# Optimization experiments

Hardware: AMD Instinct MI355X
Metric: run time of the kernel (lower is better)

The kernel has to match this reference:

```python
import jax, jax.numpy as jnp
import numpy as np

BS, L, D = 4, 2048, 1024
H, E, K = 8, 16, 2
HD = D // H            # 128
I = 4096 // H          # 512 per-expert intermediate


def setup_inputs() -> dict:
    key = jax.random.key(0)
    ks = jax.random.split(key, 10)
    s = lambda k, shp, fan: jax.random.normal(k, shp, jnp.float32) / np.sqrt(fan)
    return {
        "x": jax.random.normal(ks[0], (BS, L, D), jnp.float32),
        "Wm": s(ks[1], (D, D), D),
        "bm": jnp.zeros((D,), jnp.float32),
        "expert_emb": jax.random.normal(ks[2], (HD, E), jnp.float32),
        "W1": s(ks[3], (E, HD, I), HD),
        "b1": jnp.zeros((E, I), jnp.float32),
        "W2": s(ks[4], (E, I, HD), I),
        "b2": jnp.zeros((E, HD), jnp.float32),
        "Wo": s(ks[5], (D, D), D),
        "bo": jnp.zeros((D,), jnp.float32),
    }


def reference(x, Wm, bm, expert_emb, W1, b1, W2, b2, Wo, bo):
    bs, L_, d = x.shape
    # multi_head projection then split each token into H sub-tokens of HD dims
    h = x @ Wm + bm                              # [bs, L, d]
    t = h.reshape(bs * L_ * H, HD)               # [T, HD], T = bs*L*H
    # routing per sub-token
    logits = t @ expert_emb                      # [T, E]
    w = jax.nn.softmax(logits, axis=-1)
    topw, topi = jax.lax.top_k(w, K)             # [T, K]
    # dense all-experts MLP (faithful to torch.stack over all experts)
    hmid = jax.nn.gelu(jnp.einsum('td,edi->tei', t, W1) + b1, approximate=False)  # [T, E, I]
    eo = jnp.einsum('tei,eio->teo', hmid, W2) + b2                                # [T, E, HD]
    # gather top-k expert outputs and combine with router weights
    sel = jnp.take_along_axis(eo, topi[:, :, None], axis=1)   # [T, K, HD]
    comb = (sel * topw[:, :, None]).sum(axis=1)               # [T, HD]
    out = comb.reshape(bs, L_, d)
    return out @ Wo + bo
```

## Files before the change

### kernel.cpp

```cpp
#include <hip/hip_runtime.h>
#include <hip/hip_bf16.h>
#include <math.h>

typedef __attribute__((ext_vector_type(8))) short bx8;
typedef __attribute__((ext_vector_type(4))) short sx4;
typedef __attribute__((ext_vector_type(4))) float fx4;

#define D_   1024
#define H_   8
#define E_   16
#define HD_  128
#define I_   512
#define M8_  8192
#define T_   65536

__device__ inline float bf2f(short u) {
  unsigned int x = ((unsigned int)(unsigned short)u) << 16;
  return __builtin_bit_cast(float, x);
}
__device__ inline short f2bf(float f) {
  __hip_bfloat16 h = __float2bfloat16(f);
  return __builtin_bit_cast(short, h);
}

__device__ inline void gload_lds16(const void* g, void* l) {
  __builtin_amdgcn_global_load_lds(
      (const __attribute__((address_space(1))) void*)g,
      (__attribute__((address_space(3))) void*)l, 16, 0, 0);
}

__device__ inline fx4 mfma16(bx8 a, bx8 b, fx4 c) {
  return __builtin_amdgcn_mfma_f32_16x16x32_bf16(a, b, c, 0, 0, 0);
}

__device__ inline float gelu_erf(float x) {
  float z = fabsf(x) * 0.70710678118654752f;
  float t = __builtin_amdgcn_rcpf(fmaf(0.3275911f, z, 1.f));
  float p = t * fmaf(t, fmaf(t, fmaf(t, fmaf(t, 1.061405429f, -1.453152027f),
                                     1.421413741f), -0.284496736f), 0.254829592f);
  float er = fmaf(-p, __expf(-z * z), 1.f);
  er = copysignf(er, x);
  return 0.5f * x * (1.f + er);
}


__global__ __launch_bounds__(256) void cvt_bf16_k(const float* __restrict__ src,
                                                  __hip_bfloat16* __restrict__ dst) {
  int i = blockIdx.x * 256 + threadIdx.x;
  float4 v = *(const float4*)&src[(size_t)i * 4];
  sx4 o;
  o[0] = f2bf(v.x); o[1] = f2bf(v.y); o[2] = f2bf(v.z); o[3] = f2bf(v.w);
  *(sx4*)((short*)dst + (size_t)i * 4) = o;
}

__global__ __launch_bounds__(256) void tcvt(const float* __restrict__ src,
                                            __hip_bfloat16* __restrict__ dst,
                                            int R, int C) {
  __shared__ float tile[32][33];
  int tx = threadIdx.x & 31, ty = threadIdx.x >> 5;
  int r0 = blockIdx.y * 32, c0 = blockIdx.x * 32;
  const float* s = src + (size_t)blockIdx.z * R * C;
  __hip_bfloat16* d = dst + (size_t)blockIdx.z * R * C;
#pragma unroll
  for (int i = ty; i < 32; i += 8) tile[i][tx] = s[(size_t)(r0 + i) * C + c0 + tx];
  __syncthreads();
#pragma unroll
  for (int i = ty; i < 32; i += 8)
    d[(size_t)(c0 + i) * R + r0 + tx] = __float2bfloat16(tile[tx][i]);
}


__global__ __launch_bounds__(128) void build_wre(const float* __restrict__ Wm,
                                                 const float* __restrict__ bm,
                                                 const float* __restrict__ emb,
                                                 float* __restrict__ Wre,
                                                 float* __restrict__ rbias) {
  __shared__ float wrow[1024];
  __shared__ float embs[2048];
  int tid = threadIdx.x;
  int d = blockIdx.x;
  for (int i = tid; i < 2048; i += 128) embs[i] = emb[i];
  for (int i = tid; i < 1024; i += 128) wrow[i] = Wm[(size_t)d * 1024 + i];
  __syncthreads();
  int eta = tid >> 4, e = tid & 15;
  float acc = 0.f;
  for (int c = 0; c < 128; ++c) acc = fmaf(wrow[eta * 128 + c], embs[c * 16 + e], acc);
  Wre[(size_t)d * 128 + tid] = acc;
  if (blockIdx.x == 0) {
    float b = 0.f;
    for (int c = 0; c < 128; ++c) b = fmaf(bm[eta * 128 + c], embs[c * 16 + e], b);
    rbias[tid] = b;
  }
}

__global__ __launch_bounds__(256) void route_gemm(const float* __restrict__ x,
                                                  const float* __restrict__ Wre,
                                                  const float* __restrict__ rbias,
                                                  float* __restrict__ logits) {
  __shared__ float xs[32][128];
  int tid = threadIdx.x;
  int n = tid & 127, half = tid >> 7;
  int row0 = blockIdx.x * 32;
  float acc[16];
#pragma unroll
  for (int i = 0; i < 16; ++i) acc[i] = 0.f;
  for (int k0 = 0; k0 < 1024; k0 += 128) {
    __syncthreads();
#pragma unroll
    for (int j = 0; j < 4; ++j) {
      int i4 = tid * 4 + j * 1024;
      int row = i4 >> 7, col = i4 & 127;
      *(float4*)&xs[row][col] = *(const float4*)&x[(size_t)(row0 + row) * 1024 + k0 + col];
    }
    __syncthreads();
    for (int d4 = 0; d4 < 128; d4 += 4) {
      float w0 = Wre[(size_t)(k0 + d4 + 0) * 128 + n];
      float w1 = Wre[(size_t)(k0 + d4 + 1) * 128 + n];
      float w2 = Wre[(size_t)(k0 + d4 + 2) * 128 + n];
      float w3 = Wre[(size_t)(k0 + d4 + 3) * 128 + n];
#pragma unroll
      for (int i = 0; i < 16; ++i) {
        float4 xv = *(const float4*)&xs[half * 16 + i][d4];
        acc[i] = fmaf(xv.x, w0, acc[i]);
        acc[i] = fmaf(xv.y, w1, acc[i]);
        acc[i] = fmaf(xv.z, w2, acc[i]);
        acc[i] = fmaf(xv.w, w3, acc[i]);
      }
    }
  }
  float rb = rbias[n];
#pragma unroll
  for (int i = 0; i < 16; ++i)
    logits[(size_t)(row0 + half * 16 + i) * 128 + n] = acc[i] + rb;
}

__global__ __launch_bounds__(256) void route_topk(const float* __restrict__ logits,
                                                  float* __restrict__ topw,
                                                  int* __restrict__ list,
                                                  int* __restrict__ cnt) {
  __shared__ int lcnt[16];
  __shared__ int gbase[16];
  int tid = threadIdx.x;
  if (tid < 16) lcnt[tid] = 0;
  __syncthreads();
  int s = blockIdx.x * 256 + tid;
  const float* lp = logits + (size_t)(s >> 3) * 128 + (s & 7) * 16;
  float v[16];
#pragma unroll
  for (int j = 0; j < 4; ++j) {
    float4 t = *(const float4*)&lp[j * 4];
    v[j * 4 + 0] = t.x; v[j * 4 + 1] = t.y; v[j * 4 + 2] = t.z; v[j * 4 + 3] = t.w;
  }
  float v1 = -1e30f, v2 = -1e30f; int i1 = 0, i2 = 0;
#pragma unroll
  for (int e = 0; e < 16; ++e) {
    float val = v[e];
    if (val > v1) { v2 = v1; i2 = i1; v1 = val; i1 = e; }
    else if (val > v2) { v2 = val; i2 = e; }
  }
  float sum = 0.f;
#pragma unroll
  for (int e = 0; e < 16; ++e) sum += expf(v[e] - v1);
  topw[(size_t)2 * s + 0] = 1.0f / sum;
  topw[(size_t)2 * s + 1] = expf(v2 - v1) / sum;
  int lp1 = atomicAdd(&lcnt[i1], 1);
  int lp2 = atomicAdd(&lcnt[i2], 1);
  __syncthreads();
  if (tid < 16) gbase[tid] = atomicAdd(&cnt[tid], lcnt[tid]);
  __syncthreads();
  list[(size_t)i1 * T_ + gbase[i1] + lp1] = 2 * s;
  list[(size_t)i2 * T_ + gbase[i2] + lp2] = 2 * s + 1;
}

__global__ void prefix_k(const int* __restrict__ cnt, int* __restrict__ tileBase) {
  if (threadIdx.x == 0 && blockIdx.x == 0) {
    int s = 0;
#pragma unroll
    for (int e = 0; e < 16; ++e) { tileBase[e] = s; s += (cnt[e] + 63) >> 6; }
    tileBase[16] = s;
  }
}


template <int OUTF32>
__global__ __launch_bounds__(256) void gemm_bt(const __hip_bfloat16* __restrict__ A,
                                               const __hip_bfloat16* __restrict__ BT,
                                               const float* __restrict__ bias,
                                               void* __restrict__ Cout,
                                               int M, int N, int Kd) {
  __shared__ __hip_bfloat16 As[128 * 64];
  __shared__ __hip_bfloat16 Bs[128 * 64];
  int tid = threadIdx.x;
  int lane = tid & 63, w = tid >> 6;
  int nbn = N >> 7;
  int cpx = gridDim.x >> 3;
  int swz = (blockIdx.x & 7) * cpx + (blockIdx.x >> 3);
  int bm = swz / nbn, bn = swz % nbn;
  int wm = w >> 1, wn = w & 1;
  int r = lane & 15, g = lane >> 4;
  const fx4 fz = {0.f, 0.f, 0.f, 0.f};
  fx4 acc[4][4];
#pragma unroll
  for (int m = 0; m < 4; ++m)
#pragma unroll
    for (int n = 0; n < 4; ++n) acc[m][n] = fz;
  const short* AsS = (const short*)As;
  const short* BsS = (const short*)Bs;
  for (int k0 = 0; k0 < Kd; k0 += 64) {
    __syncthreads();
#pragma unroll
    for (int i = 0; i < 4; ++i) {
      int c = i * 256 + w * 64 + lane;
      int row = c >> 3, ko = (c & 7) * 8;
      gload_lds16(A + (size_t)(bm * 128 + row) * Kd + k0 + ko,
                  (void*)(As + (size_t)(i * 256 + w * 64) * 8));
    }
#pragma unroll
    for (int i = 0; i < 4; ++i) {
      int c = i * 256 + w * 64 + lane;
      int row = c >> 3, ko = (c & 7) * 8;
      gload_lds16(BT + (size_t)(bn * 128 + row) * Kd + k0 + ko,
                  (void*)(Bs + (size_t)(i * 256 + w * 64) * 8));
    }
    __syncthreads();
#pragma unroll
    for (int kb = 0; kb < 2; ++kb) {
      bx8 af[4], bfr[4];
#pragma unroll
      for (int m = 0; m < 4; ++m)
        af[m] = *(const bx8*)(AsS + (wm * 64 + m * 16 + r) * 64 + kb * 32 + g * 8);
#pragma unroll
      for (int n = 0; n < 4; ++n)
        bfr[n] = *(const bx8*)(BsS + (wn * 64 + n * 16 + r) * 64 + kb * 32 + g * 8);
#pragma unroll
      for (int m = 0; m < 4; ++m)
#pragma unroll
        for (int n = 0; n < 4; ++n)
          acc[m][n] = mfma16(af[m], bfr[n], acc[m][n]);
    }
  }
#pragma unroll
  for (int n = 0; n < 4; ++n) {
    int col = bn * 128 + wn * 64 + n * 16 + r;
    float bv = bias[col];
#pragma unroll
    for (int m = 0; m < 4; ++m) {
      int rowb = bm * 128 + wm * 64 + m * 16 + g * 4;
#pragma unroll
      for (int ri = 0; ri < 4; ++ri) {
        float val = acc[m][n][ri] + bv;
        if (OUTF32) ((float*)Cout)[(size_t)(rowb + ri) * N + col] = val;
        else ((__hip_bfloat16*)Cout)[(size_t)(rowb + ri) * N + col] = __float2bfloat16(val);
      }
    }
  }
}


__global__ __launch_bounds__(256, 4) void expert_mlp3(
    const __hip_bfloat16* __restrict__ h,
    const __hip_bfloat16* __restrict__ W1T,
    const __hip_bfloat16* __restrict__ W2T,
    const float* __restrict__ b1,
    const float* __restrict__ b2,
    const float* __restrict__ topw,
    const int* __restrict__ list,
    const int* __restrict__ cnt,
    const int* __restrict__ tileBase,
    __hip_bfloat16* __restrict__ eo) {
  int b = blockIdx.x;
  if (b >= tileBase[16]) return;
  int e = 0;
#pragma unroll
  for (int i = 1; i < 16; ++i) e += (b >= tileBase[i]);
  int tile = b - tileBase[e];
  int cnt_e = cnt[e];
  int base = tile * 64;
  if (base >= cnt_e) return;

  __shared__ short W1c[64 * 128];
  __shared__ short W2c[128 * 64];
  __shared__ short Hc[4 * 16 * 64];

  int tid = threadIdx.x, lane = tid & 63, wv = tid >> 6;
  int r = lane & 15, g = lane >> 4;
  const int* liste = list + (size_t)e * T_;

  int idx_own = base + wv * 16 + r;
  int p_own = (idx_own < cnt_e) ? liste[idx_own] : -1;
  const short* hS = (const short*)h;
  size_t st = (p_own >= 0) ? (size_t)(p_own >> 1) : 0;
  const short* rp = hS + st * 128 + g * 8;
  bx8 af[4];
#pragma unroll
  for (int kb = 0; kb < 4; ++kb) af[kb] = *(const bx8*)(rp + kb * 32);

  const char* W1S = (const char*)(W1T + (size_t)e * I_ * HD_);
  const char* W2S = (const char*)(W2T + (size_t)e * HD_ * I_);
  const float* b1e = b1 + (size_t)e * I_;
  const float* b2e = b2 + (size_t)e * HD_;
  char* HcW = (char*)Hc + wv * 16 * 128;

  const fx4 fz = {0.f, 0.f, 0.f, 0.f};
  fx4 acc2[8];
#pragma unroll
  for (int n = 0; n < 8; ++n) acc2[n] = fz;

  for (int c = 0; c < 8; ++c) {
    __syncthreads();
#pragma unroll
    for (int j = 0; j < 4; ++j) {
      int row = wv * 16 + j * 4 + (lane >> 4);
      int u = lane & 15;
      gload_lds16(W1S + (size_t)(c * 64 + row) * 256 + ((u * 16) ^ ((row & 7) << 4)),
                  (char*)W1c + (wv * 16 + j * 4) * 256);
    }
#pragma unroll
    for (int j = 0; j < 4; ++j) {
      int row = wv * 32 + j * 8 + (lane >> 3);
      int u = lane & 7;
      gload_lds16(W2S + (size_t)row * 1024 + c * 128 + ((u * 16) ^ ((row & 7) << 4)),
                  (char*)W2c + (wv * 32 + j * 8) * 128);
    }
    __syncthreads();

    fx4 acc1[4];
#pragma unroll
    for (int ib = 0; ib < 4; ++ib) acc1[ib] = fz;
#pragma unroll
    for (int kb = 0; kb < 4; ++kb) {
#pragma unroll
      for (int ib = 0; ib < 4; ++ib) {
        int irow = ib * 16 + r;
        bx8 a = *(const bx8*)((const char*)W1c + irow * 256 +
                              ((kb * 64 + g * 16) ^ ((irow & 7) << 4)));
        acc1[ib] = mfma16(a, af[kb], acc1[ib]);
      }
    }

#pragma unroll
    for (int ib = 0; ib < 4; ++ib) {
      float4 b1v = *(const float4*)&b1e[c * 64 + ib * 16 + g * 4];
      sx4 ov;
      ov[0] = f2bf(gelu_erf(acc1[ib][0] + b1v.x));
      ov[1] = f2bf(gelu_erf(acc1[ib][1] + b1v.y));
      ov[2] = f2bf(gelu_erf(acc1[ib][2] + b1v.z));
      ov[3] = f2bf(gelu_erf(acc1[ib][3] + b1v.w));
      *(sx4*)(HcW + r * 128 + ((ib * 32 + g * 8) ^ ((r & 7) << 4))) = ov;
    }

#pragma unroll
    for (int kb2 = 0; kb2 < 2; ++kb2) {
      bx8 ha = *(const bx8*)(HcW + r * 128 + ((kb2 * 64 + g * 16) ^ ((r & 7) << 4)));
#pragma unroll
      for (int ob = 0; ob < 8; ++ob) {
        int orow = ob * 16 + r;
        bx8 wb = *(const bx8*)((const char*)W2c + orow * 128 +
                               ((kb2 * 64 + g * 16) ^ ((orow & 7) << 4)));
        acc2[ob] = mfma16(ha, wb, acc2[ob]);
      }
    }
  }

  int pid_ep[4];
  float wt_ep[4];
#pragma unroll
  for (int ri = 0; ri < 4; ++ri) {
    int idx = base + wv * 16 + g * 4 + ri;
    int p = (idx < cnt_e) ? liste[idx] : -1;
    pid_ep[ri] = p;
    wt_ep[ri] = (p >= 0) ? topw[p] : 0.f;
  }
#pragma unroll
  for (int ob = 0; ob < 8; ++ob) {
    float b2v = b2e[ob * 16 + r];
#pragma unroll
    for (int ri = 0; ri < 4; ++ri) {
      int p = pid_ep[ri];
      if (p >= 0) {
        float v = (acc2[ob][ri] + b2v) * wt_ep[ri];
        eo[(size_t)p * 128 + ob * 16 + r] = __float2bfloat16(v);
      }
    }
  }
}

__global__ __launch_bounds__(256) void combine_k(const __hip_bfloat16* __restrict__ eo,
                                                 __hip_bfloat16* __restrict__ comb) {
  int t = blockIdx.x * 256 + threadIdx.x;
  int s = t >> 4, oo = (t & 15) * 8;
  const short* eS = (const short*)eo;
  bx8 a = *(const bx8*)(eS + (size_t)s * 256 + oo);
  bx8 b = *(const bx8*)(eS + (size_t)s * 256 + 128 + oo);
  bx8 ov;
#pragma unroll
  for (int j = 0; j < 8; ++j) ov[j] = f2bf(bf2f(a[j]) + bf2f(b[j]));
  *(bx8*)((short*)comb + (size_t)s * 128 + oo) = ov;
}


extern "C" void kernel_launch(void* const* d_in, const int* in_sizes, int n_in,
                              void* d_out, int out_size, void* d_ws, size_t ws_size,
                              hipStream_t stream) {
  const float* x   = (const float*)d_in[0];
  const float* Wm  = (const float*)d_in[1];
  const float* bm  = (const float*)d_in[2];
  const float* emb = (const float*)d_in[3];
  const float* W1  = (const float*)d_in[4];
  const float* b1  = (const float*)d_in[5];
  const float* W2  = (const float*)d_in[6];
  const float* b2  = (const float*)d_in[7];
  const float* Wo  = (const float*)d_in[8];
  const float* bo  = (const float*)d_in[9];

  char* ws = (char*)d_ws;
  size_t off = 0;
  auto alloc = [&](size_t b) { size_t r = off; off += (b + 255) & ~(size_t)255; return r; };
  __hip_bfloat16* xb   = (__hip_bfloat16*)(ws + alloc((size_t)M8_ * D_ * 2));
  __hip_bfloat16* WmT  = (__hip_bfloat16*)(ws + alloc((size_t)D_ * D_ * 2));
  __hip_bfloat16* WoT  = (__hip_bfloat16*)(ws + alloc((size_t)D_ * D_ * 2));
  __hip_bfloat16* W1T  = (__hip_bfloat16*)(ws + alloc((size_t)E_ * HD_ * I_ * 2));
  __hip_bfloat16* W2T  = (__hip_bfloat16*)(ws + alloc((size_t)E_ * HD_ * I_ * 2));
  __hip_bfloat16* hb   = (__hip_bfloat16*)(ws + alloc((size_t)M8_ * D_ * 2));
  float* Wre    = (float*)(ws + alloc((size_t)D_ * 128 * 4));
  float* rbias  = (float*)(ws + alloc(512));
  float* logits = (float*)(ws + alloc((size_t)T_ * 16 * 4));
  float* topw   = (float*)(ws + alloc((size_t)T_ * 2 * 4));
  int*   cnt    = (int*)(ws + alloc(256));
  int*   tileBase = (int*)(ws + alloc(256));
  int*   list   = (int*)(ws + alloc((size_t)E_ * T_ * 4));
  __hip_bfloat16* eo   = (__hip_bfloat16*)(ws + alloc((size_t)T_ * 2 * HD_ * 2));
  __hip_bfloat16* comb = (__hip_bfloat16*)(ws + alloc((size_t)M8_ * D_ * 2));

  hipMemsetAsync(cnt, 0, 256, stream);
  cvt_bf16_k<<<8192, 256, 0, stream>>>(x, xb);
  tcvt<<<dim3(32, 32, 1), 256, 0, stream>>>(Wm, WmT, 1024, 1024);
  tcvt<<<dim3(32, 32, 1), 256, 0, stream>>>(Wo, WoT, 1024, 1024);
  tcvt<<<dim3(16, 4, 16), 256, 0, stream>>>(W1, W1T, 128, 512);
  tcvt<<<dim3(4, 16, 16), 256, 0, stream>>>(W2, W2T, 512, 128);
  build_wre<<<1024, 128, 0, stream>>>(Wm, bm, emb, Wre, rbias);
  gemm_bt<0><<<512, 256, 0, stream>>>(xb, WmT, bm, hb, M8_, D_, D_);
  route_gemm<<<256, 256, 0, stream>>>(x, Wre, rbias, logits);
  route_topk<<<256, 256, 0, stream>>>(logits, topw, list, cnt);
  prefix_k<<<1, 32, 0, stream>>>(cnt, tileBase);
  expert_mlp3<<<2064, 256, 0, stream>>>(hb, W1T, W2T, b1, b2, topw, list, cnt,
                                        tileBase, eo);
  combine_k<<<4096, 256, 0, stream>>>(eo, comb);
  gemm_bt<1><<<512, 256, 0, stream>>>(comb, WoT, bo, d_out, M8_, D_, D_);
}
```

Measured before the change: 405.7 us.

## Fuse routing GEMM with top-k selection and stage Wre in shared memory

```diff
diff --git a/kernel.cpp b/kernel.cpp
--- a/kernel.cpp
+++ b/kernel.cpp
@@ -93,34 +93,46 @@
   }
 }
 
-__global__ __launch_bounds__(256) void route_gemm(const float* __restrict__ x,
-                                                  const float* __restrict__ Wre,
-                                                  const float* __restrict__ rbias,
-                                                  float* __restrict__ logits) {
-  __shared__ float xs[32][128];
+__global__ __launch_bounds__(256) void route_fused(const float* __restrict__ x,
+                                                   const float* __restrict__ Wre,
+                                                   const float* __restrict__ rbias,
+                                                   float* __restrict__ topw,
+                                                   int* __restrict__ list,
+                                                   int* __restrict__ cnt) {
+  __shared__ float xs[16][64];
+  __shared__ float wsh[64][128];
+  __shared__ float ls[16][129];
+  __shared__ int lcnt[16];
+  __shared__ int gbase[16];
   int tid = threadIdx.x;
   int n = tid & 127, half = tid >> 7;
-  int row0 = blockIdx.x * 32;
-  float acc[16];
-#pragma unroll
-  for (int i = 0; i < 16; ++i) acc[i] = 0.f;
-  for (int k0 = 0; k0 < 1024; k0 += 128) {
-    __syncthreads();
-#pragma unroll
-    for (int j = 0; j < 4; ++j) {
+  int row0 = blockIdx.x * 16;
+  if (tid < 16) lcnt[tid] = 0;
+  float acc[8];
+#pragma unroll
+  for (int i = 0; i < 8; ++i) acc[i] = 0.f;
+
+  for (int k0 = 0; k0 < 1024; k0 += 64) {
+    __syncthreads();
+    {
+      int i4 = tid * 4;
+      int row = i4 >> 6, col = i4 & 63;
+      *(float4*)&xs[row][col] = *(const float4*)&x[(size_t)(row0 + row) * 1024 + k0 + col];
+    }
+#pragma unroll
+    for (int j = 0; j < 8; ++j) {
       int i4 = tid * 4 + j * 1024;
       int row = i4 >> 7, col = i4 & 127;
-      *(float4*)&xs[row][col] = *(const float4*)&x[(size_t)(row0 + row) * 1024 + k0 + col];
-    }
-    __syncthreads();
-    for (int d4 = 0; d4 < 128; d4 += 4) {
-      float w0 = Wre[(size_t)(k0 + d4 + 0) * 128 + n];
-      float w1 = Wre[(size_t)(k0 + d4 + 1) * 128 + n];
-      float w2 = Wre[(size_t)(k0 + d4 + 2) * 128 + n];
-      float w3 = Wre[(size_t)(k0 + d4 + 3) * 128 + n];
-#pragma unroll
-      for (int i = 0; i < 16; ++i) {
-        float4 xv = *(const float4*)&xs[half * 16 + i][d4];
+      *(float4*)&wsh[row][col] = *(const float4*)&Wre[(size_t)(k0 + row) * 128 + col];
+    }
+    __syncthreads();
+#pragma unroll 4
+    for (int d4 = 0; d4 < 64; d4 += 4) {
+      float w0 = wsh[d4 + 0][n], w1 = wsh[d4 + 1][n];
+      float w2 = wsh[d4 + 2][n], w3 = wsh[d4 + 3][n];
+#pragma unroll
+      for (int i = 0; i < 8; ++i) {
+        float4 xv = *(const float4*)&xs[half * 8 + i][d4];
         acc[i] = fmaf(xv.x, w0, acc[i]);
         acc[i] = fmaf(xv.y, w1, acc[i]);
         acc[i] = fmaf(xv.z, w2, acc[i]);
@@ -130,46 +142,38 @@
   }
   float rb = rbias[n];
 #pragma unroll
-  for (int i = 0; i < 16; ++i)
-    logits[(size_t)(row0 + half * 16 + i) * 128 + n] = acc[i] + rb;
-}
-
-__global__ __launch_bounds__(256) void route_topk(const float* __restrict__ logits,
-                                                  float* __restrict__ topw,
-                                                  int* __restrict__ list,
-                                                  int* __restrict__ cnt) {
-  __shared__ int lcnt[16];
-  __shared__ int gbase[16];
-  int tid = threadIdx.x;
-  if (tid < 16) lcnt[tid] = 0;
+  for (int i = 0; i < 8; ++i) ls[half * 8 + i][n] = acc[i] + rb;
   __syncthreads();
-  int s = blockIdx.x * 256 + tid;
-  const float* lp = logits + (size_t)(s >> 3) * 128 + (s & 7) * 16;
-  float v[16];
-#pragma unroll
-  for (int j = 0; j < 4; ++j) {
-    float4 t = *(const float4*)&lp[j * 4];
-    v[j * 4 + 0] = t.x; v[j * 4 + 1] = t.y; v[j * 4 + 2] = t.z; v[j * 4 + 3] = t.w;
-  }
-  float v1 = -1e30f, v2 = -1e30f; int i1 = 0, i2 = 0;
-#pragma unroll
-  for (int e = 0; e < 16; ++e) {
-    float val = v[e];
-    if (val > v1) { v2 = v1; i2 = i1; v1 = val; i1 = e; }
-    else if (val > v2) { v2 = val; i2 = e; }
-  }
-  float sum = 0.f;
-#pragma unroll
-  for (int e = 0; e < 16; ++e) sum += expf(v[e] - v1);
-  topw[(size_t)2 * s + 0] = 1.0f / sum;
-  topw[(size_t)2 * s + 1] = expf(v2 - v1) / sum;
-  int lp1 = atomicAdd(&lcnt[i1], 1);
-  int lp2 = atomicAdd(&lcnt[i2], 1);
+
+  int i1 = 0, i2 = 0, lp1 = 0, lp2 = 0, s = 0;
+  if (tid < 128) {
+    int lr = tid >> 3, eta = tid & 7;
+    s = (row0 + lr) * 8 + eta;
+    float v[16];
+#pragma unroll
+    for (int e = 0; e < 16; ++e) v[e] = ls[lr][eta * 16 + e];
+    float v1 = -1e30f, v2 = -1e30f;
+#pragma unroll
+    for (int e = 0; e < 16; ++e) {
+      float val = v[e];
+      if (val > v1) { v2 = v1; i2 = i1; v1 = val; i1 = e; }
+      else if (val > v2) { v2 = val; i2 = e; }
+    }
+    float sum = 0.f;
+#pragma unroll
+    for (int e = 0; e < 16; ++e) sum += expf(v[e] - v1);
+    topw[(size_t)2 * s + 0] = 1.0f / sum;
+    topw[(size_t)2 * s + 1] = expf(v2 - v1) / sum;
+    lp1 = atomicAdd(&lcnt[i1], 1);
+    lp2 = atomicAdd(&lcnt[i2], 1);
+  }
   __syncthreads();
   if (tid < 16) gbase[tid] = atomicAdd(&cnt[tid], lcnt[tid]);
   __syncthreads();
-  list[(size_t)i1 * T_ + gbase[i1] + lp1] = 2 * s;
-  list[(size_t)i2 * T_ + gbase[i2] + lp2] = 2 * s + 1;
+  if (tid < 128) {
+    list[(size_t)i1 * T_ + gbase[i1] + lp1] = 2 * s;
+    list[(size_t)i2 * T_ + gbase[i2] + lp2] = 2 * s + 1;
+  }
 }
 
 __global__ void prefix_k(const int* __restrict__ cnt, int* __restrict__ tileBase) {
@@ -424,7 +428,6 @@
   __hip_bfloat16* hb   = (__hip_bfloat16*)(ws + alloc((size_t)M8_ * D_ * 2));
   float* Wre    = (float*)(ws + alloc((size_t)D_ * 128 * 4));
   float* rbias  = (float*)(ws + alloc(512));
-  float* logits = (float*)(ws + alloc((size_t)T_ * 16 * 4));
   float* topw   = (float*)(ws + alloc((size_t)T_ * 2 * 4));
   int*   cnt    = (int*)(ws + alloc(256));
   int*   tileBase = (int*)(ws + alloc(256));
@@ -440,8 +443,7 @@
   tcvt<<<dim3(4, 16, 16), 256, 0, stream>>>(W2, W2T, 512, 128);
   build_wre<<<1024, 128, 0, stream>>>(Wm, bm, emb, Wre, rbias);
   gemm_bt<0><<<512, 256, 0, stream>>>(xb, WmT, bm, hb, M8_, D_, D_);
-  route_gemm<<<256, 256, 0, stream>>>(x, Wre, rbias, logits);
-  route_topk<<<256, 256, 0, stream>>>(logits, topw, list, cnt);
+  route_fused<<<512, 256, 0, stream>>>(x, Wre, rbias, topw, list, cnt);
   prefix_k<<<1, 32, 0, stream>>>(cnt, tileBase);
   expert_mlp3<<<2064, 256, 0, stream>>>(hb, W1T, W2T, b1, b2, topw, list, cnt,
                                         tileBase, eo);
```

New measurement: 362.0 us. -10.8%, faster.
